# Kernel optimization log

Measured on AMD Instinct MI355X. Metric: run time of the kernel, lower is better.

Reference implementation:

```python
import jax, jax.numpy as jnp
import numpy as np

N = 50000        # num nodes
E = 800000       # num edges (before self loops)
IN = 256         # in_channels
H = 4            # heads
C = 32           # out_channels per head
NEG_SLOPE = 0.2


def _glorot(key, shape):
    fan = shape[-2] * (shape[-1] if len(shape) > 2 else 1) + shape[-1]
    # PyG glorot: uniform(-s, s) with s = sqrt(6 / (fan_in + fan_out))
    s = float(np.sqrt(6.0 / (shape[-2] + shape[-1])))
    return jax.random.uniform(key, shape, jnp.float32, -s, s)


def setup_inputs() -> dict:
    key = jax.random.key(0)
    k1, k2, k3, k4, k5 = jax.random.split(key, 5)
    x = jax.random.normal(k1, (N, IN), jnp.float32)
    src = jax.random.randint(k2, (E,), 0, N)
    dst = jax.random.randint(k3, (E,), 0, N)
    # guarantee no self loops (module removes them then re-adds exactly N loops)
    dst = jnp.where(dst == src, (dst + 1) % N, dst)
    edge_index = jnp.stack([src, dst]).astype(jnp.int32)
    weight = _glorot(k4, (IN, H * C))
    att = _glorot(k5, (1, H, 2 * C))
    bias = jnp.zeros((H * C,), jnp.float32)
    return {"x": x, "weight": weight, "att": att, "bias": bias,
            "edge_index": edge_index}


def reference(x, weight, att, bias, edge_index):
    n = x.shape[0]
    # linear projection -> [N, H, C]
    h = (x @ weight).reshape(n, H, C)
    # add self loops (input edge_index has none)
    loops = jnp.arange(n, dtype=edge_index.dtype)
    ei = jnp.concatenate([edge_index, jnp.stack([loops, loops])], axis=1)
    src, dst = ei[0], ei[1]          # flow source_to_target: j=src(row 0), i=dst(row 1)
    x_j = h[src]                     # [E', H, C] source features
    x_i = h[dst]                     # [E', H, C] target features
    wl = att[:, :, :C]               # applied to x_i (first half of concat)
    wr = att[:, :, C:]               # applied to x_j
    alpha = (x_i * wl).sum(-1) + (x_j * wr).sum(-1)   # [E', H]
    alpha = jax.nn.leaky_relu(alpha, NEG_SLOPE)
    # NOTE: module normalizes softmax over edge_index[0] (src) segments
    seg = src
    amax = jax.ops.segment_max(alpha, seg, num_segments=n)
    alpha = jnp.exp(alpha - amax[seg])
    denom = jax.ops.segment_sum(alpha, seg, num_segments=n)
    alpha = alpha / (denom[seg] + 1e-16)
    # weighted messages, aggregated at edge_index[i] = edge_index[1] (dst)
    msg = x_j * alpha[:, :, None]                     # [E', H, C]
    out = jax.ops.segment_sum(msg, dst, num_segments=n)  # [N, H, C]
    return out.reshape(n, H * C) + bias
```

## Files before the change

kernel.cpp:

```cpp
#include <hip/hip_runtime.h>
#include <hip/hip_fp16.h>
#include <math.h>


#define NH 4
#define CH 32
#define HC 128
#define IND 256
#define NEG_SLOPE 0.2f
#define CSH 8
#define NCB_MAX 256
#define CHUNK 4096
#define BCAP 6144

typedef __attribute__((ext_vector_type(8))) short bf16x8;
typedef __attribute__((ext_vector_type(16))) float f32x16;

__device__ __forceinline__ unsigned short f2bf(float f) {
    unsigned int u = __float_as_uint(f);
    unsigned int r = (u + 0x7FFFu + ((u >> 16) & 1u)) >> 16;
    return (unsigned short)r;
}
__device__ __forceinline__ float bf2f(unsigned short s) {
    return __uint_as_float(((unsigned int)s) << 16);
}

__global__ __launch_bounds__(256) void k_wprep(const float* __restrict__ W,
                                               unsigned short* __restrict__ WT_bf,
                                               int* __restrict__ gcurS,
                                               int* __restrict__ gcurD) {
    int t = blockIdx.x * 256 + threadIdx.x;
    if (blockIdx.x == 0) { gcurS[threadIdx.x] = 0; gcurD[threadIdx.x] = 0; }
    if (t < IND * HC) {
        int c = t >> 8;
        int k = t & 255;
        WT_bf[t] = f2bf(W[k * HC + c]);
    }
}

__global__ __launch_bounds__(512) void k_gs(const float* __restrict__ x,
                                            const unsigned short* __restrict__ WT_bf,
                                            const float* __restrict__ att,
                                            unsigned short* __restrict__ h_bf,
                                            float* __restrict__ al,
                                            float* __restrict__ ar,
                                            const int* __restrict__ ei,
                                            int* __restrict__ gcurS,
                                            int* __restrict__ gcurD,
                                            unsigned int* __restrict__ recS,
                                            unsigned int* __restrict__ recD,
                                            int E, int NE, int ncb, int nsb, int N) {
    __shared__ float cs[128 * 132];

    const int tid = threadIdx.x;

    if (blockIdx.x < nsb) {
        unsigned int* srt = (unsigned int*)cs;
        int* cnt  = (int*)(srt + CHUNK);
        int* off  = cnt + NCB_MAX;
        int* cur  = off + NCB_MAX;
        int* gpos = cur + NCB_MAX;
        int* sc   = gpos + NCB_MAX;

        const int t0 = blockIdx.x * CHUNK;
        const int m  = min(CHUNK, NE - t0);

        unsigned int myrec[8];
        unsigned int mvalm = 0;
#pragma unroll
        for (int j = 0; j < 8; j++) {
            int i = j * 512 + tid;
            int t = t0 + i;
            int src = 0, dst = 0;
            if (i < m) {
                mvalm |= 1u << j;
                if (t < E) { src = ei[t]; dst = ei[E + t]; }
                else       { src = dst = t - E; }
            }
            myrec[j] = (unsigned int)src | ((unsigned int)dst << 16);
        }

        for (int side = 0; side < 2; side++) {
            if (tid < 256) cnt[tid] = 0;
            __syncthreads();
            int mybkt[8];
#pragma unroll
            for (int j = 0; j < 8; j++) {
                unsigned int r = myrec[j];
                int node = side ? (int)(r >> 16) : (int)(r & 0xFFFFu);
                mybkt[j] = node >> CSH;
                if (mvalm & (1u << j)) atomicAdd(&cnt[mybkt[j]], 1);
            }
            __syncthreads();
            int v = (tid < 256) ? cnt[tid] : 0;
            if (tid < 256) sc[tid] = v;
            __syncthreads();
            for (int o = 1; o < 256; o <<= 1) {
                int t = (tid >= o && tid < 256) ? sc[tid - o] : 0;
                __syncthreads();
                if (tid < 256) sc[tid] += t;
                __syncthreads();
            }
            if (tid < 256) { off[tid] = sc[tid] - v; cur[tid] = sc[tid] - v; }
            __syncthreads();
#pragma unroll
            for (int j = 0; j < 8; j++) {
                if (mvalm & (1u << j)) {
                    int p = atomicAdd(&cur[mybkt[j]], 1);
                    srt[p] = myrec[j];
                }
            }
            __syncthreads();
            int* gcur = side ? gcurD : gcurS;
            if (tid < ncb) {
                int c = cnt[tid];
                gpos[tid] = c ? atomicAdd(&gcur[tid], c) : 0;
            }
            __syncthreads();
            unsigned int* recX = side ? recD : recS;
            for (int i = tid; i < m; i += 512) {
                unsigned int r = srt[i];
                int node = side ? (int)(r >> 16) : (int)(r & 0xFFFFu);
                int cb = node >> CSH;
                int p  = gpos[cb] + (i - off[cb]);
                if (p < BCAP)
                    recX[(size_t)cb * BCAP + p] = r;
            }
            __syncthreads();
        }
        return;
    }

    unsigned short* xs  = (unsigned short*)cs;
    unsigned short* wsP = (unsigned short*)cs + 17408;

    const int row0 = (blockIdx.x - nsb) * 256;
    const int wave = tid >> 6;
    const int lane = tid & 63;
    const int n32  = lane & 31;
    const int half = lane >> 5;

    float4 xv[8];
    int4   wv0, wv1;

#define XLOAD(p)                                                             \
    {                                                                        \
        _Pragma("unroll")                                                    \
        for (int j = 0; j < 8; j++) {                                        \
            int fid = j * 512 + tid;                                         \
            int gr  = row0 + (fid >> 4);                                     \
            float4 t = make_float4(0.f, 0.f, 0.f, 0.f);                      \
            if (gr < N)                                                      \
                t = *(const float4*)(x + (size_t)gr * IND + (p) * 64 +       \
                                     (fid & 15) * 4);                        \
            xv[j] = t;                                                       \
        }                                                                    \
    }
#define WLOAD(p)                                                             \
    {                                                                        \
        const unsigned short* wp = WT_bf + (tid >> 2) * IND + (p) * 64 +     \
                                   (tid & 3) * 16;                           \
        wv0 = *(const int4*)wp;                                              \
        wv1 = *(const int4*)(wp + 8);                                        \
    }
#define XWRITE()                                                             \
    {                                                                        \
        _Pragma("unroll")                                                    \
        for (int j = 0; j < 8; j++) {                                        \
            int fid = j * 512 + tid;                                         \
            int row = fid >> 4;                                              \
            ushort4 o;                                                       \
            o.x = f2bf(xv[j].x); o.y = f2bf(xv[j].y);                        \
            o.z = f2bf(xv[j].z); o.w = f2bf(xv[j].w);                        \
            *(ushort4*)(xs + row * 68 + (fid & 15) * 4) = o;                 \
        }                                                                    \
    }
#define WWRITE()                                                             \
    {                                                                        \
        unsigned short* wq = wsP + (tid >> 2) * 68 + (tid & 3) * 16;         \
        *(int4*)wq       = wv0;                                              \
        *(int4*)(wq + 8) = wv1;                                              \
    }

    XLOAD(0); WLOAD(0);

    f32x16 acc[4];
#pragma unroll
    for (int t = 0; t < 4; t++)
#pragma unroll
        for (int r = 0; r < 16; r++) acc[t][r] = 0.0f;

    const int arow = wave * 32 + n32;
#pragma unroll
    for (int p = 0; p < 4; p++) {
        __syncthreads();
        XWRITE(); WWRITE();
        __syncthreads();
        if (p < 3) { XLOAD(p + 1); WLOAD(p + 1); }
#pragma unroll
        for (int s = 0; s < 4; s++) {
            bf16x8 a = *(const bf16x8*)(xs + arow * 68 + s * 16 + half * 8);
#pragma unroll
            for (int t = 0; t < 4; t++) {
                bf16x8 b = *(const bf16x8*)(wsP + (t * 32 + n32) * 68 +
                                            s * 16 + half * 8);
                acc[t] = __builtin_amdgcn_mfma_f32_32x32x16_bf16(a, b, acc[t], 0, 0, 0);
            }
        }
    }
#undef XLOAD
#undef WLOAD
#undef XWRITE
#undef WWRITE
    __syncthreads();

    for (int pass = 0; pass < 2; pass++) {
        if ((wave >> 2) == pass) {
            const int lw = wave & 3;
#pragma unroll
            for (int t = 0; t < 4; t++)
#pragma unroll
                for (int r = 0; r < 16; r++) {
                    int rl = lw * 32 + (r & 3) + 8 * (r >> 2) + 4 * half;
                    cs[rl * 132 + t * 33 + n32] = acc[t][r];
                }
        }
        __syncthreads();

        const int rl   = tid >> 2;
        const int hq   = tid & 3;
        const int orow = row0 + pass * 128 + rl;
        if (orow < N) {
            const float* cr = cs + rl * 132 + hq * 33;
            unsigned short* hp = h_bf + (size_t)orow * HC + hq * CH;
#pragma unroll
            for (int c = 0; c < 32; c += 8) {
                ushort4 o0, o1;
                o0.x = f2bf(cr[c]);     o0.y = f2bf(cr[c + 1]);
                o0.z = f2bf(cr[c + 2]); o0.w = f2bf(cr[c + 3]);
                o1.x = f2bf(cr[c + 4]); o1.y = f2bf(cr[c + 5]);
                o1.z = f2bf(cr[c + 6]); o1.w = f2bf(cr[c + 7]);
                *(ushort4*)(hp + c) = o0;
                *(ushort4*)(hp + c + 4) = o1;
            }
            const float* w0 = att + hq * (2 * CH);
            float sl = 0.f, sr = 0.f;
#pragma unroll
            for (int c = 0; c < CH; c++) {
                float v2 = cr[c];
                sl += v2 * w0[c];
                sr += v2 * w0[CH + c];
            }
            al[orow * NH + hq] = sl;
            ar[orow * NH + hq] = sr;
        }
        __syncthreads();
    }
}

__global__ __launch_bounds__(256) void k_bucket(const unsigned int* __restrict__ recS,
                                                const unsigned int* __restrict__ recD,
                                                const int* __restrict__ gcurS,
                                                const int* __restrict__ gcurD,
                                                const float* __restrict__ al,
                                                const float* __restrict__ ar,
                                                unsigned short* __restrict__ adjD,
                                                int* __restrict__ rowB,
                                                int* __restrict__ rowE,
                                                float* __restrict__ arw,
                                                int ncb, int N) {
    __shared__ int cnt[256], cur[256], sc[256];
    __shared__ float lsums[256 * NH];
    __shared__ float lar[256 * NH];
    const int tid = threadIdx.x;

    if (blockIdx.x < ncb) {
        const int cb = blockIdx.x;
        const int b0 = cb * BCAP;
        const int tot_rec = min(gcurD[cb], BCAP);

        cnt[tid] = 0;
        __syncthreads();
        for (int i = tid; i < tot_rec; i += 256) {
            unsigned int r = recD[b0 + i];
            atomicAdd(&cnt[(r >> 16) & 255], 1);
        }
        __syncthreads();
        int v = cnt[tid];
        sc[tid] = v;
        __syncthreads();
        for (int o = 1; o < 256; o <<= 1) {
            int t = (tid >= o) ? sc[tid - o] : 0;
            __syncthreads();
            sc[tid] += t;
            __syncthreads();
        }
        int ex = sc[tid] - v;
        int node_g = (cb << CSH) + tid;
        if (node_g < N) { rowB[node_g] = b0 + ex; rowE[node_g] = b0 + ex + v; }
        cur[tid] = ex;
        __syncthreads();
        for (int i = tid; i < tot_rec; i += 256) {
            unsigned int r = recD[b0 + i];
            int node = (int)(r >> 16) & 255;
            int p = atomicAdd(&cur[node], 1);
            adjD[b0 + p] = (unsigned short)(r & 0xFFFFu);
        }
    } else {
        const int cb = blockIdx.x - ncb;
        const int b0 = cb * BCAP;
        const int b1 = b0 + min(gcurS[cb], BCAP);
        const int node_g = (cb << CSH) + tid;

        float4 arv = make_float4(0.f, 0.f, 0.f, 0.f);
        if (node_g < N) arv = *(const float4*)(ar + (size_t)node_g * NH);
        *(float4*)(lar + tid * NH) = arv;
        *(float4*)(lsums + tid * NH) = make_float4(0.f, 0.f, 0.f, 0.f);
        __syncthreads();

        int i = b0 + tid;
        for (; i + 256 < b1; i += 512) {
            unsigned int r0 = recS[i];
            unsigned int r1 = recS[i + 256];
            int sl0 = (int)(r0 & 255u), dst0 = (int)(r0 >> 16);
            int sl1 = (int)(r1 & 255u), dst1 = (int)(r1 >> 16);
            float4 av0 = *(const float4*)(al + (size_t)dst0 * NH);
            float4 av1 = *(const float4*)(al + (size_t)dst1 * NH);
            const float* w0 = lar + sl0 * NH;
            const float* w1 = lar + sl1 * NH;
            float a0 = av0.x + w0[0], a1 = av0.y + w0[1];
            float a2 = av0.z + w0[2], a3 = av0.w + w0[3];
            float c0 = av1.x + w1[0], c1 = av1.y + w1[1];
            float c2 = av1.z + w1[2], c3 = av1.w + w1[3];
            a0 = (a0 > 0.f) ? a0 : NEG_SLOPE * a0;
            a1 = (a1 > 0.f) ? a1 : NEG_SLOPE * a1;
            a2 = (a2 > 0.f) ? a2 : NEG_SLOPE * a2;
            a3 = (a3 > 0.f) ? a3 : NEG_SLOPE * a3;
            c0 = (c0 > 0.f) ? c0 : NEG_SLOPE * c0;
            c1 = (c1 > 0.f) ? c1 : NEG_SLOPE * c1;
            c2 = (c2 > 0.f) ? c2 : NEG_SLOPE * c2;
            c3 = (c3 > 0.f) ? c3 : NEG_SLOPE * c3;
            float* s0 = lsums + sl0 * NH;
            float* s1 = lsums + sl1 * NH;
            atomicAdd(s0 + 0, __expf(a0));
            atomicAdd(s0 + 1, __expf(a1));
            atomicAdd(s0 + 2, __expf(a2));
            atomicAdd(s0 + 3, __expf(a3));
            atomicAdd(s1 + 0, __expf(c0));
            atomicAdd(s1 + 1, __expf(c1));
            atomicAdd(s1 + 2, __expf(c2));
            atomicAdd(s1 + 3, __expf(c3));
        }
        if (i < b1) {
            unsigned int r = recS[i];
            int slot = (int)(r & 255u);
            int dst  = (int)(r >> 16);
            float4 alv = *(const float4*)(al + (size_t)dst * NH);
            const float* av = lar + slot * NH;
            float a0 = alv.x + av[0], a1 = alv.y + av[1];
            float a2 = alv.z + av[2], a3 = alv.w + av[3];
            a0 = (a0 > 0.f) ? a0 : NEG_SLOPE * a0;
            a1 = (a1 > 0.f) ? a1 : NEG_SLOPE * a1;
            a2 = (a2 > 0.f) ? a2 : NEG_SLOPE * a2;
            a3 = (a3 > 0.f) ? a3 : NEG_SLOPE * a3;
            float* sp = lsums + slot * NH;
            atomicAdd(sp + 0, __expf(a0));
            atomicAdd(sp + 1, __expf(a1));
            atomicAdd(sp + 2, __expf(a2));
            atomicAdd(sp + 3, __expf(a3));
        }
        __syncthreads();

        if (node_g < N) {
            const float* sp = lsums + tid * NH;
            float4 p0 = make_float4(arv.x, 1.0f / (sp[0] + 1e-16f),
                                    arv.y, 1.0f / (sp[1] + 1e-16f));
            float4 p1 = make_float4(arv.z, 1.0f / (sp[2] + 1e-16f),
                                    arv.w, 1.0f / (sp[3] + 1e-16f));
            *(float4*)(arw + (size_t)node_g * 8)     = p0;
            *(float4*)(arw + (size_t)node_g * 8 + 4) = p1;
        }
    }
}

__global__ __launch_bounds__(256) void k_agg(const int* __restrict__ rowB,
                                             const int* __restrict__ rowE,
                                             const unsigned short* __restrict__ adjD,
                                             const float* __restrict__ al,
                                             const float* __restrict__ arw,
                                             const unsigned short* __restrict__ h_bf,
                                             const float* __restrict__ bias,
                                             float* __restrict__ out, int N) {
    const int g = threadIdx.x >> 5;
    const int n = blockIdx.x * 8 + g;
    if (n >= N) return;
    const int l  = threadIdx.x & 31;
    const int c0 = l * 4;
    const int hh = l >> 3;
    const int beg = rowB[n], end = rowE[n];
    const float alv = al[n * NH + hh];

    float a0 = 0.f, a1 = 0.f, a2 = 0.f, a3 = 0.f;

    for (int base = beg; base < end; base += 32) {
        int idx = base + l;
        int av  = (idx < end) ? (int)adjD[idx] : 0;
        int cnt = min(32, end - base);
        int e = 0;
        for (; e + 4 <= cnt; e += 4) {
            int s0 = __shfl(av, e,     32);
            int s1 = __shfl(av, e + 1, 32);
            int s2 = __shfl(av, e + 2, 32);
            int s3 = __shfl(av, e + 3, 32);
            ushort4 u0 = *(const ushort4*)(h_bf + (size_t)s0 * HC + c0);
            ushort4 u1 = *(const ushort4*)(h_bf + (size_t)s1 * HC + c0);
            ushort4 u2 = *(const ushort4*)(h_bf + (size_t)s2 * HC + c0);
            ushort4 u3 = *(const ushort4*)(h_bf + (size_t)s3 * HC + c0);
            float2 p0 = *(const float2*)(arw + (size_t)s0 * 8 + hh * 2);
            float2 p1 = *(const float2*)(arw + (size_t)s1 * 8 + hh * 2);
            float2 p2 = *(const float2*)(arw + (size_t)s2 * 8 + hh * 2);
            float2 p3 = *(const float2*)(arw + (size_t)s3 * 8 + hh * 2);
            float t0 = alv + p0.x; t0 = (t0 > 0.f) ? t0 : NEG_SLOPE * t0;
            float t1 = alv + p1.x; t1 = (t1 > 0.f) ? t1 : NEG_SLOPE * t1;
            float t2 = alv + p2.x; t2 = (t2 > 0.f) ? t2 : NEG_SLOPE * t2;
            float t3 = alv + p3.x; t3 = (t3 > 0.f) ? t3 : NEG_SLOPE * t3;
            float w0 = __expf(t0) * p0.y;
            float w1 = __expf(t1) * p1.y;
            float w2 = __expf(t2) * p2.y;
            float w3 = __expf(t3) * p3.y;
            a0 += bf2f(u0.x) * w0; a1 += bf2f(u0.y) * w0;
            a2 += bf2f(u0.z) * w0; a3 += bf2f(u0.w) * w0;
            a0 += bf2f(u1.x) * w1; a1 += bf2f(u1.y) * w1;
            a2 += bf2f(u1.z) * w1; a3 += bf2f(u1.w) * w1;
            a0 += bf2f(u2.x) * w2; a1 += bf2f(u2.y) * w2;
            a2 += bf2f(u2.z) * w2; a3 += bf2f(u2.w) * w2;
            a0 += bf2f(u3.x) * w3; a1 += bf2f(u3.y) * w3;
            a2 += bf2f(u3.z) * w3; a3 += bf2f(u3.w) * w3;
        }
        for (; e < cnt; e++) {
            int s0 = __shfl(av, e, 32);
            ushort4 u0 = *(const ushort4*)(h_bf + (size_t)s0 * HC + c0);
            float2 p0 = *(const float2*)(arw + (size_t)s0 * 8 + hh * 2);
            float t0 = alv + p0.x; t0 = (t0 > 0.f) ? t0 : NEG_SLOPE * t0;
            float w0 = __expf(t0) * p0.y;
            a0 += bf2f(u0.x) * w0; a1 += bf2f(u0.y) * w0;
            a2 += bf2f(u0.z) * w0; a3 += bf2f(u0.w) * w0;
        }
    }
    float4 b4 = *(const float4*)(bias + c0);
    *(float4*)(out + (size_t)n * HC + c0) =
        make_float4(a0 + b4.x, a1 + b4.y, a2 + b4.z, a3 + b4.w);
}

extern "C" void kernel_launch(void* const* d_in, const int* in_sizes, int n_in,
                              void* d_out, int out_size, void* d_ws, size_t ws_size,
                              hipStream_t stream) {
    const float* x    = (const float*)d_in[0];
    const float* W    = (const float*)d_in[1];
    const float* att  = (const float*)d_in[2];
    const float* bias = (const float*)d_in[3];
    const int*   ei   = (const int*)d_in[4];

    const int N  = in_sizes[0] / IND;
    const int E  = in_sizes[4] / 2;
    const int NE = E + N;
    const int ncb = (N + (1 << CSH) - 1) >> CSH;
    const int nsb = (NE + CHUNK - 1) / CHUNK;
    const int ngb = (N + 255) / 256;
    float* out = (float*)d_out;
    const int nodeTot = N * NH;
    const size_t capTot = (size_t)ncb * BCAP;

    unsigned short* h_bf  = (unsigned short*)d_ws;
    unsigned short* WT_bf = h_bf + (size_t)N * HC;
    float* al   = (float*)(WT_bf + IND * HC);
    float* ar   = al + nodeTot;
    float* arw  = ar + nodeTot;
    unsigned int* recS = (unsigned int*)(arw + (size_t)N * 8);
    unsigned int* recD = recS + capTot;
    unsigned short* adjD = (unsigned short*)(recD + capTot);
    int* rowB    = (int*)(adjD + capTot + (capTot & 1));
    int* rowE    = rowB + N;
    int* gcurS   = rowE + N;
    int* gcurD   = gcurS + NCB_MAX;

    k_wprep<<<(IND * HC + 255) / 256, 256, 0, stream>>>(W, WT_bf, gcurS, gcurD);
    k_gs<<<nsb + ngb, 512, 0, stream>>>(x, WT_bf, att, h_bf, al, ar, ei,
                                        gcurS, gcurD, recS, recD,
                                        E, NE, ncb, nsb, N);
    k_bucket<<<2 * ncb, 256, 0, stream>>>(recS, recD, gcurS, gcurD, al, ar,
                                          adjD, rowB, rowE, arw, ncb, N);
    k_agg<<<(N + 7) / 8, 256, 0, stream>>>(rowB, rowE, adjD, al, arw, h_bf,
                                           bias, out, N);
}
```

Before: 208.6 us.

## Split fused scatter/GEMM kernel into separate scatter and GEMM launches

Replaces the combined kernel, in which some blocks bucketed edges and others ran the projection GEMM, with two kernels. The new scatter kernel uses 256 threads and a much smaller LDS footprint than the GEMM's 66KB buffer, so more scatter blocks can be resident at once. It computes src and dst histograms in one pass and replaces the barrier-heavy shared-memory scan with wave shuffle scans. The cost is an extra launch and the loss of overlap between the scatter and GEMM work, which now run one after the other on the stream.

```diff
diff --git a/kernel.cpp b/kernel.cpp
--- a/kernel.cpp
+++ b/kernel.cpp
@@ -38,103 +38,123 @@
     }
 }
 
-__global__ __launch_bounds__(512) void k_gs(const float* __restrict__ x,
-                                            const unsigned short* __restrict__ WT_bf,
-                                            const float* __restrict__ att,
-                                            unsigned short* __restrict__ h_bf,
-                                            float* __restrict__ al,
-                                            float* __restrict__ ar,
-                                            const int* __restrict__ ei,
-                                            int* __restrict__ gcurS,
-                                            int* __restrict__ gcurD,
-                                            unsigned int* __restrict__ recS,
-                                            unsigned int* __restrict__ recD,
-                                            int E, int NE, int ncb, int nsb, int N) {
+__global__ __launch_bounds__(256) void k_scatter(const int* __restrict__ ei,
+                                                 int* __restrict__ gcurS,
+                                                 int* __restrict__ gcurD,
+                                                 unsigned int* __restrict__ recS,
+                                                 unsigned int* __restrict__ recD,
+                                                 int E, int NE, int ncb) {
+    __shared__ unsigned int srt[CHUNK];
+    __shared__ int cntS[256], cntD[256];
+    __shared__ int offS[256], offD[256];
+    __shared__ int curSl[256], curDl[256];
+    __shared__ int gposS[256], gposD[256];
+    __shared__ int wsumS[4], wsumD[4];
+
+    const int tid  = threadIdx.x;
+    const int lane = tid & 63;
+    const int wv   = tid >> 6;
+    const int t0   = blockIdx.x * CHUNK;
+    const int m    = min(CHUNK, NE - t0);
+
+    cntS[tid] = 0; cntD[tid] = 0;
+
+    unsigned int myrec[16];
+    unsigned int mval = 0;
+#pragma unroll
+    for (int j = 0; j < 16; j++) {
+        int i = j * 256 + tid;
+        int t = t0 + i;
+        int src = 0, dst = 0;
+        if (i < m) {
+            mval |= 1u << j;
+            if (t < E) { src = ei[t]; dst = ei[E + t]; }
+            else       { src = dst = t - E; }
+        }
+        myrec[j] = (unsigned int)src | ((unsigned int)dst << 16);
+    }
+    __syncthreads();
+
+#pragma unroll
+    for (int j = 0; j < 16; j++) {
+        if (mval & (1u << j)) {
+            unsigned int r = myrec[j];
+            atomicAdd(&cntS[(r & 0xFFFFu) >> CSH], 1);
+            atomicAdd(&cntD[(r >> 16) >> CSH], 1);
+        }
+    }
+    __syncthreads();
+
+    int vS = cntS[tid], vD = cntD[tid];
+    int sS = vS, sD = vD;
+#pragma unroll
+    for (int d = 1; d < 64; d <<= 1) {
+        int tS = __shfl_up(sS, d, 64);
+        int tD = __shfl_up(sD, d, 64);
+        if (lane >= d) { sS += tS; sD += tD; }
+    }
+    if (lane == 63) { wsumS[wv] = sS; wsumD[wv] = sD; }
+    __syncthreads();
+    int baseS = 0, baseD = 0;
+    for (int w = 0; w < wv; w++) { baseS += wsumS[w]; baseD += wsumD[w]; }
+    int exS = baseS + sS - vS;
+    int exD = baseD + sD - vD;
+    offS[tid] = exS; curSl[tid] = exS;
+    offD[tid] = exD; curDl[tid] = exD;
+    if (tid < ncb) {
+        gposS[tid] = vS ? atomicAdd(&gcurS[tid], vS) : 0;
+        gposD[tid] = vD ? atomicAdd(&gcurD[tid], vD) : 0;
+    }
+    __syncthreads();
+
+#pragma unroll
+    for (int j = 0; j < 16; j++) {
+        if (mval & (1u << j)) {
+            unsigned int r = myrec[j];
+            int p = atomicAdd(&curSl[(r & 0xFFFFu) >> CSH], 1);
+            srt[p] = r;
+        }
+    }
+    __syncthreads();
+    for (int i = tid; i < m; i += 256) {
+        unsigned int r = srt[i];
+        int cb = (int)(r & 0xFFFFu) >> CSH;
+        int p  = gposS[cb] + (i - offS[cb]);
+        if (p < BCAP)
+            recS[(size_t)cb * BCAP + p] = r;
+    }
+    __syncthreads();
+
+#pragma unroll
+    for (int j = 0; j < 16; j++) {
+        if (mval & (1u << j)) {
+            unsigned int r = myrec[j];
+            int p = atomicAdd(&curDl[(r >> 16) >> CSH], 1);
+            srt[p] = r;
+        }
+    }
+    __syncthreads();
+    for (int i = tid; i < m; i += 256) {
+        unsigned int r = srt[i];
+        int cb = (int)(r >> 16) >> CSH;
+        int p  = gposD[cb] + (i - offD[cb]);
+        if (p < BCAP)
+            recD[(size_t)cb * BCAP + p] = r;
+    }
+}
+
+__global__ __launch_bounds__(512) void k_gemm(const float* __restrict__ x,
+                                              const unsigned short* __restrict__ WT_bf,
+                                              const float* __restrict__ att,
+                                              unsigned short* __restrict__ h_bf,
+                                              float* __restrict__ al,
+                                              float* __restrict__ ar, int N) {
     __shared__ float cs[128 * 132];
-
-    const int tid = threadIdx.x;
-
-    if (blockIdx.x < nsb) {
-        unsigned int* srt = (unsigned int*)cs;
-        int* cnt  = (int*)(srt + CHUNK);
-        int* off  = cnt + NCB_MAX;
-        int* cur  = off + NCB_MAX;
-        int* gpos = cur + NCB_MAX;
-        int* sc   = gpos + NCB_MAX;
-
-        const int t0 = blockIdx.x * CHUNK;
-        const int m  = min(CHUNK, NE - t0);
-
-        unsigned int myrec[8];
-        unsigned int mvalm = 0;
-#pragma unroll
-        for (int j = 0; j < 8; j++) {
-            int i = j * 512 + tid;
-            int t = t0 + i;
-            int src = 0, dst = 0;
-            if (i < m) {
-                mvalm |= 1u << j;
-                if (t < E) { src = ei[t]; dst = ei[E + t]; }
-                else       { src = dst = t - E; }
-            }
-            myrec[j] = (unsigned int)src | ((unsigned int)dst << 16);
-        }
-
-        for (int side = 0; side < 2; side++) {
-            if (tid < 256) cnt[tid] = 0;
-            __syncthreads();
-            int mybkt[8];
-#pragma unroll
-            for (int j = 0; j < 8; j++) {
-                unsigned int r = myrec[j];
-                int node = side ? (int)(r >> 16) : (int)(r & 0xFFFFu);
-                mybkt[j] = node >> CSH;
-                if (mvalm & (1u << j)) atomicAdd(&cnt[mybkt[j]], 1);
-            }
-            __syncthreads();
-            int v = (tid < 256) ? cnt[tid] : 0;
-            if (tid < 256) sc[tid] = v;
-            __syncthreads();
-            for (int o = 1; o < 256; o <<= 1) {
-                int t = (tid >= o && tid < 256) ? sc[tid - o] : 0;
-                __syncthreads();
-                if (tid < 256) sc[tid] += t;
-                __syncthreads();
-            }
-            if (tid < 256) { off[tid] = sc[tid] - v; cur[tid] = sc[tid] - v; }
-            __syncthreads();
-#pragma unroll
-            for (int j = 0; j < 8; j++) {
-                if (mvalm & (1u << j)) {
-                    int p = atomicAdd(&cur[mybkt[j]], 1);
-                    srt[p] = myrec[j];
-                }
-            }
-            __syncthreads();
-            int* gcur = side ? gcurD : gcurS;
-            if (tid < ncb) {
-                int c = cnt[tid];
-                gpos[tid] = c ? atomicAdd(&gcur[tid], c) : 0;
-            }
-            __syncthreads();
-            unsigned int* recX = side ? recD : recS;
-            for (int i = tid; i < m; i += 512) {
-                unsigned int r = srt[i];
-                int node = side ? (int)(r >> 16) : (int)(r & 0xFFFFu);
-                int cb = node >> CSH;
-                int p  = gpos[cb] + (i - off[cb]);
-                if (p < BCAP)
-                    recX[(size_t)cb * BCAP + p] = r;
-            }
-            __syncthreads();
-        }
-        return;
-    }
-
     unsigned short* xs  = (unsigned short*)cs;
     unsigned short* wsP = (unsigned short*)cs + 17408;
 
-    const int row0 = (blockIdx.x - nsb) * 256;
+    const int tid  = threadIdx.x;
+    const int row0 = blockIdx.x * 256;
     const int wave = tid >> 6;
     const int lane = tid & 63;
     const int n32  = lane & 31;
@@ -485,9 +505,8 @@
     int* gcurD   = gcurS + NCB_MAX;
 
     k_wprep<<<(IND * HC + 255) / 256, 256, 0, stream>>>(W, WT_bf, gcurS, gcurD);
-    k_gs<<<nsb + ngb, 512, 0, stream>>>(x, WT_bf, att, h_bf, al, ar, ei,
-                                        gcurS, gcurD, recS, recD,
-                                        E, NE, ncb, nsb, N);
+    k_scatter<<<nsb, 256, 0, stream>>>(ei, gcurS, gcurD, recS, recD, E, NE, ncb);
+    k_gemm<<<ngb, 512, 0, stream>>>(x, WT_bf, att, h_bf, al, ar, N);
     k_bucket<<<2 * ncb, 256, 0, stream>>>(recS, recD, gcurS, gcurD, al, ar,
                                           adjD, rowB, rowE, arw, ncb, N);
     k_agg<<<(N + 7) / 8, 256, 0, stream>>>(rowB, rowE, adjD, al, arw, h_bf,
```

New measurement: 218.3 us. +4.6%, slower.
